# Performance work log

Measured on AMD Instinct MI355X. Metric: run time of the kernel, lower is better.

The kernel has to match this reference:

```python
import jax, jax.numpy as jnp
import numpy as np

N_NODES = 50000
DIM = 64
HEADS = 4
N_EDGES = 800000
NEG_SLOPE = 0.2  # PyG GATConv default


def setup_inputs() -> dict:
    key = jax.random.key(0)
    ks = jax.random.split(key, 8)
    H, C = HEADS, DIM
    embedding = jax.random.normal(ks[0], (N_NODES, DIM), dtype=jnp.float32)
    graph = jax.random.randint(ks[1], (2, N_EDGES), 0, N_NODES, dtype=jnp.int64)
    s = 1.0 / np.sqrt(DIM)
    # GATConv params: shared source/target linear (PyG uses one lin when in_channels is int)
    W = jax.random.normal(ks[2], (DIM, H * C), dtype=jnp.float32) * s
    att_src = jax.random.normal(ks[3], (H, C), dtype=jnp.float32) * s
    att_dst = jax.random.normal(ks[4], (H, C), dtype=jnp.float32) * s
    bias = jnp.zeros((H * C,), dtype=jnp.float32)
    # dense: Linear(dim*heads -> dim)
    dense_w = jax.random.normal(ks[5], (H * C, DIM), dtype=jnp.float32) / np.sqrt(H * C)
    dense_b = jnp.zeros((DIM,), dtype=jnp.float32)
    return {"embedding": embedding, "graph": graph, "W": W, "att_src": att_src,
            "att_dst": att_dst, "bias": bias, "dense_w": dense_w, "dense_b": dense_b}


def reference(embedding, graph, W, att_src, att_dst, bias, dense_w, dense_b):
    N, D = embedding.shape
    H, C = att_src.shape
    # linear projection, per-head view: [N, H, C]
    x = (embedding @ W).reshape(N, H, C)
    # add self loops (PyG default add_self_loops=True)
    ar = jnp.arange(N, dtype=graph.dtype)
    src = jnp.concatenate([graph[0], ar])  # [E+N]
    dst = jnp.concatenate([graph[1], ar])
    # per-node attention logits, gathered per edge
    a_src = jnp.einsum('nhc,hc->nh', x, att_src)  # [N, H]
    a_dst = jnp.einsum('nhc,hc->nh', x, att_dst)
    alpha = jax.nn.leaky_relu(a_src[src] + a_dst[dst], NEG_SLOPE)  # [E, H]
    # segment softmax over destination nodes
    amax = jax.ops.segment_max(alpha, dst, num_segments=N)  # [N, H]
    amax = jnp.where(jnp.isfinite(amax), amax, 0.0)
    ex = jnp.exp(alpha - amax[dst])
    denom = jax.ops.segment_sum(ex, dst, num_segments=N)
    coef = ex / (denom[dst] + 1e-16)  # [E, H]
    # weighted scatter-aggregate of source features
    msg = x[src] * coef[:, :, None]  # [E, H, C]
    agg = jax.ops.segment_sum(msg, dst, num_segments=N)  # [N, H, C]
    gat_out = agg.reshape(N, H * C) + bias  # concat heads + bias
    return gat_out @ dense_w + dense_b  # [N, D]
```

## Files before the change

### kernel.cpp

```cpp
#include <hip/hip_runtime.h>
#include <hip/hip_fp16.h>
#include <cfloat>
#include <cmath>

#define DIM 64
#define HEADS 4
#define NEG 0.2f
#define CAP 64
#define NPART 8
#define BPP 96

typedef int v4i __attribute__((ext_vector_type(4)));

__device__ __forceinline__ float lrelu(float a) { return a > 0.0f ? a : NEG * a; }

__device__ __forceinline__ unsigned pack_half2(float a, float b) {
    return (unsigned)__half_as_ushort(__float2half(a)) |
           ((unsigned)__half_as_ushort(__float2half(b)) << 16);
}

__global__ __launch_bounds__(256) void prep_kernel(
        const float* __restrict__ W, const float* __restrict__ dw,
        const float* __restrict__ att_s, const float* __restrict__ att_d,
        const float* __restrict__ bias, const float* __restrict__ db,
        const float* __restrict__ emb,
        float* __restrict__ M, float* __restrict__ bvec,
        float* __restrict__ a_src, float* __restrict__ a_dst,
        int* __restrict__ cnt, int N) {
    const int b = blockIdx.x, t = threadIdx.x;
    if (b < 64) {
        __shared__ float s_W[256];
        s_W[t] = W[b * 256 + t];
        __syncthreads();
        const int h = t >> 6, j = t & 63;
        float s = 0.f;
        for (int c = 0; c < 64; c++)
            s = fmaf(s_W[h * 64 + c], dw[(h * 64 + c) * 64 + j], s);
        M[b * 256 + t] = s;
    } else if (b == 64) {
        __shared__ float s_p[256];
        const int j = t & 63, kq = t >> 6;
        float p = 0.f;
        for (int k = kq * 64; k < kq * 64 + 64; k++)
            p = fmaf(bias[k], dw[k * 64 + j], p);
        s_p[t] = p;
        __syncthreads();
        if (t < 64)
            bvec[t] = s_p[t] + s_p[64 + t] + s_p[128 + t] + s_p[192 + t] + db[t];
    } else {
        __shared__ float s_e[64 * 68];
        __shared__ float s_vs[256], s_vd[256];
        const int n0 = (b - 65) * 64;
        {
            const int d = t >> 2, h = t & 3;
            const float4* w4 = (const float4*)(W + d * 256 + h * 64);
            const float4* s4 = (const float4*)(att_s + h * 64);
            const float4* d4 = (const float4*)(att_d + h * 64);
            float vs = 0.f, vd = 0.f;
#pragma unroll
            for (int k = 0; k < 16; k++) {
                float4 w = w4[k], as = s4[k], ad = d4[k];
                vs = fmaf(w.x, as.x, fmaf(w.y, as.y, fmaf(w.z, as.z, fmaf(w.w, as.w, vs))));
                vd = fmaf(w.x, ad.x, fmaf(w.y, ad.y, fmaf(w.z, ad.z, fmaf(w.w, ad.w, vd))));
            }
            s_vs[h * 64 + d] = vs;
            s_vd[h * 64 + d] = vd;
        }
#pragma unroll
        for (int r = 0; r < 4; r++) {
            int idx = (r * 256 + t) * 4;
            int i = idx >> 6, d = idx & 63;
            int row = min(n0 + i, N - 1);
            *(float4*)(s_e + i * 68 + d) = *(const float4*)(emb + (size_t)row * 64 + d);
        }
        __syncthreads();
        const int node = t >> 2, h = t & 3;
        const float* er = s_e + node * 68;
        float as = 0.f, ad = 0.f;
#pragma unroll
        for (int g = 0; g < 16; g++) {
            float4 ev = *(const float4*)(er + 4 * g);
            float4 vs = *(const float4*)(s_vs + h * 64 + 4 * g);
            float4 vd = *(const float4*)(s_vd + h * 64 + 4 * g);
            as = fmaf(ev.x, vs.x, fmaf(ev.y, vs.y, fmaf(ev.z, vs.z, fmaf(ev.w, vs.w, as))));
            ad = fmaf(ev.x, vd.x, fmaf(ev.y, vd.y, fmaf(ev.z, vd.z, fmaf(ev.w, vd.w, ad))));
        }
        const int n = n0 + node;
        if (n < N) {
            a_src[(size_t)n * 4 + h] = as;
            a_dst[(size_t)n * 4 + h] = ad;
        }
        if (t < 64 && n0 + t < N) cnt[n0 + t] = 0;
    }
}

__global__ __launch_bounds__(256) void project_kernel(
        const float* __restrict__ emb, const float* __restrict__ M,
        unsigned* __restrict__ y32, int N) {
    __shared__ float s_e[64 * 68];
    const int t = threadIdx.x;
    const int l = t & 63;
    const int wq = __builtin_amdgcn_readfirstlane(t >> 6);
    const int n0 = blockIdx.x * 64;

#pragma unroll
    for (int r = 0; r < 4; r++) {
        int idx = (r * 256 + t) * 4;
        int i = idx >> 6, d = idx & 63;
        int row = min(n0 + i, N - 1);
        *(float4*)(s_e + i * 68 + d) = *(const float4*)(emb + (size_t)row * 64 + d);
    }
    __syncthreads();

    float4 acc[16];
#pragma unroll
    for (int i = 0; i < 16; i++) acc[i] = make_float4(0.f, 0.f, 0.f, 0.f);

    const float* eb = s_e + wq * 16 * 68;

    for (int g = 0; g < 16; g++) {
        const int d0 = g * 4;
        float4 wv0 = *(const float4*)(M + (d0 + 0) * 256 + 4 * l);
        float4 wv1 = *(const float4*)(M + (d0 + 1) * 256 + 4 * l);
        float4 wv2 = *(const float4*)(M + (d0 + 2) * 256 + 4 * l);
        float4 wv3 = *(const float4*)(M + (d0 + 3) * 256 + 4 * l);
#pragma unroll
        for (int i = 0; i < 16; i++) {
            float4 ev = *(const float4*)(eb + i * 68 + d0);
            acc[i].x = fmaf(ev.x, wv0.x, acc[i].x);
            acc[i].y = fmaf(ev.x, wv0.y, acc[i].y);
            acc[i].z = fmaf(ev.x, wv0.z, acc[i].z);
            acc[i].w = fmaf(ev.x, wv0.w, acc[i].w);
            acc[i].x = fmaf(ev.y, wv1.x, acc[i].x);
            acc[i].y = fmaf(ev.y, wv1.y, acc[i].y);
            acc[i].z = fmaf(ev.y, wv1.z, acc[i].z);
            acc[i].w = fmaf(ev.y, wv1.w, acc[i].w);
            acc[i].x = fmaf(ev.z, wv2.x, acc[i].x);
            acc[i].y = fmaf(ev.z, wv2.y, acc[i].y);
            acc[i].z = fmaf(ev.z, wv2.z, acc[i].z);
            acc[i].w = fmaf(ev.z, wv2.w, acc[i].w);
            acc[i].x = fmaf(ev.w, wv3.x, acc[i].x);
            acc[i].y = fmaf(ev.w, wv3.y, acc[i].y);
            acc[i].z = fmaf(ev.w, wv3.z, acc[i].z);
            acc[i].w = fmaf(ev.w, wv3.w, acc[i].w);
        }
    }

#pragma unroll
    for (int i = 0; i < 16; i++) {
        int n = n0 + wq * 16 + i;
        if (n < N) {
            unsigned long long u =
                (unsigned long long)pack_half2(acc[i].x, acc[i].y) |
                ((unsigned long long)pack_half2(acc[i].z, acc[i].w) << 32);
            __builtin_nontemporal_store(u,
                (unsigned long long*)(y32 + (size_t)n * 128 + 2 * l));
        }
    }
}

__global__ __launch_bounds__(256) void fill_kernel(
        const int* __restrict__ gsrc, const int* __restrict__ gdst,
        int* __restrict__ cnt, int* __restrict__ adj, int E, int N) {
    const int t = threadIdx.x;
    const int part = blockIdx.x & (NPART - 1);
    const int slot = blockIdx.x >> 3;
    const int lo = (int)((long long)part * N / NPART);
    const int hi = (int)((long long)(part + 1) * N / NPART);
    const unsigned span = (unsigned)(hi - lo);
    const int quads = (E + 3) >> 2;
    const int stride = BPP * 256;

    for (int q = slot * 256 + t; q < quads; q += stride) {
        const int e0 = q * 4;
        v4i s4, d4;
        if (e0 + 3 < E) {
            d4 = __builtin_nontemporal_load((const v4i*)(gdst + e0));
            s4 = __builtin_nontemporal_load((const v4i*)(gsrc + e0));
        } else {
#pragma unroll
            for (int k = 0; k < 4; k++) {
                const int e = e0 + k;
                d4[k] = (e < E) ? gdst[e] : -1;
                s4[k] = (e < E) ? gsrc[e] : 0;
            }
        }
#pragma unroll
        for (int k = 0; k < 4; k++) {
            const int d = d4[k];
            if ((unsigned)(d - lo) < span) {
                const int pos = atomicAdd(&cnt[d], 1);
                if (pos < CAP) adj[(size_t)d * CAP + pos] = s4[k];
            }
        }
    }
}

__global__ __launch_bounds__(256) void aggregate_kernel(
        const int* __restrict__ cnt, const int* __restrict__ adj,
        const float* __restrict__ a_src, const float* __restrict__ a_dst,
        const unsigned* __restrict__ y32, const float* __restrict__ bvec,
        float* __restrict__ out, int N) {
    const int t = threadIdx.x;
    const int l = t & 63;
    const int dd = blockIdx.x * 4 + (t >> 6);
    if (dd >= N) return;
    const int d = __builtin_amdgcn_readfirstlane(dd);
    const int hl = l >> 4;
    const int lh = l & 48;
    const int deg = min(__builtin_amdgcn_readfirstlane(cnt[d]), CAP);
    const unsigned* yl = y32 + 2 * l;

    int my_src = 0;
    if (l < deg) my_src = adj[(size_t)d * CAP + l];

    const float ad = a_dst[(size_t)d * 4 + hl];

    float pv0, pv1, pv2, pv3;
    {
        const int q = l & 15;
#define PRE_PV(G, PV) {                                                    \
            const int e_ = (G) * 16 + q;                                   \
            const int se_ = __shfl(my_src, e_, 64);                        \
            float pe_ = 0.f;                                               \
            if (e_ < deg)                                                  \
                pe_ = __expf(lrelu(a_src[(size_t)se_ * 4 + hl] + ad));     \
            (PV) = pe_; }
        PRE_PV(0, pv0); PRE_PV(1, pv1); PRE_PV(2, pv2); PRE_PV(3, pv3);
#undef PRE_PV
    }

    float den, ax, ay, az, aw;
    {
        const float p = __expf(lrelu(a_src[(size_t)d * 4 + hl] + ad));
        const uint2 v = *(const uint2*)(yl + (size_t)d * 128);
        const float2 f0 = __half22float2(*(const __half2*)&v.x);
        const float2 f1 = __half22float2(*(const __half2*)&v.y);
        den = p;
        ax = p * f0.x; ay = p * f0.y; az = p * f1.x; aw = p * f1.y;
    }

#define AGG_EDGE(PG, I, J) {                                               \
        const int si_ = __builtin_amdgcn_readlane(my_src, (I));            \
        const float pe_ = __shfl((PG), lh + (J), 64);                      \
        const uint2 vv_ = *(const uint2*)(yl + (size_t)si_ * 128);         \
        const float2 g0_ = __half22float2(*(const __half2*)&vv_.x);        \
        const float2 g1_ = __half22float2(*(const __half2*)&vv_.y);        \
        den += pe_;                                                        \
        ax = fmaf(pe_, g0_.x, ax); ay = fmaf(pe_, g0_.y, ay);              \
        az = fmaf(pe_, g1_.x, az); aw = fmaf(pe_, g1_.y, aw); }

#define AGG_GROUP(G, PG) {                                                 \
        const int base_ = (G) * 16;                                        \
        if (base_ < deg) {                                                 \
            const int mp_ = min(16, ((deg - base_) + 3) & ~3);             \
            _Pragma("unroll 1")                                            \
            for (int j = 0; j < mp_; j += 4) {                             \
                AGG_EDGE(PG, base_ + j + 0, j + 0);                        \
                AGG_EDGE(PG, base_ + j + 1, j + 1);                        \
                AGG_EDGE(PG, base_ + j + 2, j + 2);                        \
                AGG_EDGE(PG, base_ + j + 3, j + 3);                        \
            }                                                              \
        } }

    AGG_GROUP(0, pv0);
    AGG_GROUP(1, pv1);
    AGG_GROUP(2, pv2);
    AGG_GROUP(3, pv3);
#undef AGG_GROUP
#undef AGG_EDGE

    const float inv = 1.0f / (den + 1e-16f);
    float rx = ax * inv, ry = ay * inv, rz = az * inv, rw = aw * inv;
    rx += __shfl_xor(rx, 16, 64); ry += __shfl_xor(ry, 16, 64);
    rz += __shfl_xor(rz, 16, 64); rw += __shfl_xor(rw, 16, 64);
    rx += __shfl_xor(rx, 32, 64); ry += __shfl_xor(ry, 32, 64);
    rz += __shfl_xor(rz, 32, 64); rw += __shfl_xor(rw, 32, 64);
    if (l < 16) {
        float4 bv = *(const float4*)(bvec + 4 * l);
        float4 r;
        r.x = rx + bv.x; r.y = ry + bv.y; r.z = rz + bv.z; r.w = rw + bv.w;
        *(float4*)(out + (size_t)dd * 64 + 4 * l) = r;
    }
}

extern "C" void kernel_launch(void* const* d_in, const int* in_sizes, int n_in,
                              void* d_out, int out_size, void* d_ws, size_t ws_size,
                              hipStream_t stream) {
    const float* emb   = (const float*)d_in[0];
    const int*   graph = (const int*)d_in[1];
    const float* W     = (const float*)d_in[2];
    const float* att_s = (const float*)d_in[3];
    const float* att_d = (const float*)d_in[4];
    const float* bias  = (const float*)d_in[5];
    const float* dw    = (const float*)d_in[6];
    const float* db    = (const float*)d_in[7];
    float* out = (float*)d_out;

    const int N = in_sizes[0] / DIM;
    const int E = in_sizes[1] / 2;
    const int* gsrc = graph;
    const int* gdst = graph + E;

    unsigned* y32  = (unsigned*)d_ws;
    int* adj       = (int*)(y32 + (size_t)N * 128);
    float* a_src   = (float*)(adj + (size_t)N * CAP);
    float* a_dst   = a_src + (size_t)N * 4;
    float* M       = a_dst + (size_t)N * 4;
    float* bvec    = M + 64 * 256;
    int*   cnt     = (int*)(bvec + 64);

    const int PB = (N + 63) / 64;
    const int FILLB = NPART * BPP;

    hipLaunchKernelGGL(prep_kernel, dim3(65 + PB), dim3(256), 0, stream,
                       W, dw, att_s, att_d, bias, db, emb,
                       M, bvec, a_src, a_dst, cnt, N);
    hipLaunchKernelGGL(project_kernel, dim3(PB), dim3(256), 0, stream,
                       emb, M, y32, N);
    hipLaunchKernelGGL(fill_kernel, dim3(FILLB), dim3(256), 0, stream,
                       gsrc, gdst, cnt, adj, E, N);
    hipLaunchKernelGGL(aggregate_kernel, dim3((N + 3) / 4), dim3(256), 0, stream,
                       cnt, adj, a_src, a_dst, y32, bvec, out, N);
}
```

Measured before the change: 228.0 us.

## Aggregate raw fp16 embeddings per head, then apply fused projection after aggregation

Moves the combined W·dense_w projection from before the edge aggregation to after it. The aggregate kernel now gathers 64-dim fp16 embeddings (128 B per source) instead of 256-dim projected features (512 B per source), and writes per-head weighted embeddings to a buffer. A new output GEMM kernel multiplies that buffer by the per-head fused matrix. This cuts gather traffic in the edge loop at the cost of an extra intermediate buffer write/read and a larger post-aggregation GEMM.

```diff
diff --git a/kernel.cpp b/kernel.cpp
--- a/kernel.cpp
+++ b/kernel.cpp
@@ -24,9 +24,9 @@
         const float* __restrict__ att_s, const float* __restrict__ att_d,
         const float* __restrict__ bias, const float* __restrict__ db,
         const float* __restrict__ emb,
-        float* __restrict__ M, float* __restrict__ bvec,
+        __half* __restrict__ M2h, float* __restrict__ bvec,
         float* __restrict__ a_src, float* __restrict__ a_dst,
-        int* __restrict__ cnt, int N) {
+        unsigned* __restrict__ embh, int* __restrict__ cnt, int N) {
     const int b = blockIdx.x, t = threadIdx.x;
     if (b < 64) {
         __shared__ float s_W[256];
@@ -36,7 +36,7 @@
         float s = 0.f;
         for (int c = 0; c < 64; c++)
             s = fmaf(s_W[h * 64 + c], dw[(h * 64 + c) * 64 + j], s);
-        M[b * 256 + t] = s;
+        M2h[(size_t)(h * 64 + b) * 64 + j] = __float2half(s);
     } else if (b == 64) {
         __shared__ float s_p[256];
         const int j = t & 63, kq = t >> 6;
@@ -89,73 +89,17 @@
         if (n < N) {
             a_src[(size_t)n * 4 + h] = as;
             a_dst[(size_t)n * 4 + h] = ad;
+            const float* ep = s_e + node * 68 + h * 16;
+            uint4 u0, u1;
+            u0.x = pack_half2(ep[0],  ep[1]);  u0.y = pack_half2(ep[2],  ep[3]);
+            u0.z = pack_half2(ep[4],  ep[5]);  u0.w = pack_half2(ep[6],  ep[7]);
+            u1.x = pack_half2(ep[8],  ep[9]);  u1.y = pack_half2(ep[10], ep[11]);
+            u1.z = pack_half2(ep[12], ep[13]); u1.w = pack_half2(ep[14], ep[15]);
+            unsigned* dst = embh + (size_t)n * 32 + h * 8;
+            *(uint4*)dst = u0;
+            *(uint4*)(dst + 4) = u1;
         }
         if (t < 64 && n0 + t < N) cnt[n0 + t] = 0;
-    }
-}
-
-__global__ __launch_bounds__(256) void project_kernel(
-        const float* __restrict__ emb, const float* __restrict__ M,
-        unsigned* __restrict__ y32, int N) {
-    __shared__ float s_e[64 * 68];
-    const int t = threadIdx.x;
-    const int l = t & 63;
-    const int wq = __builtin_amdgcn_readfirstlane(t >> 6);
-    const int n0 = blockIdx.x * 64;
-
-#pragma unroll
-    for (int r = 0; r < 4; r++) {
-        int idx = (r * 256 + t) * 4;
-        int i = idx >> 6, d = idx & 63;
-        int row = min(n0 + i, N - 1);
-        *(float4*)(s_e + i * 68 + d) = *(const float4*)(emb + (size_t)row * 64 + d);
-    }
-    __syncthreads();
-
-    float4 acc[16];
-#pragma unroll
-    for (int i = 0; i < 16; i++) acc[i] = make_float4(0.f, 0.f, 0.f, 0.f);
-
-    const float* eb = s_e + wq * 16 * 68;
-
-    for (int g = 0; g < 16; g++) {
-        const int d0 = g * 4;
-        float4 wv0 = *(const float4*)(M + (d0 + 0) * 256 + 4 * l);
-        float4 wv1 = *(const float4*)(M + (d0 + 1) * 256 + 4 * l);
-        float4 wv2 = *(const float4*)(M + (d0 + 2) * 256 + 4 * l);
-        float4 wv3 = *(const float4*)(M + (d0 + 3) * 256 + 4 * l);
-#pragma unroll
-        for (int i = 0; i < 16; i++) {
-            float4 ev = *(const float4*)(eb + i * 68 + d0);
-            acc[i].x = fmaf(ev.x, wv0.x, acc[i].x);
-            acc[i].y = fmaf(ev.x, wv0.y, acc[i].y);
-            acc[i].z = fmaf(ev.x, wv0.z, acc[i].z);
-            acc[i].w = fmaf(ev.x, wv0.w, acc[i].w);
-            acc[i].x = fmaf(ev.y, wv1.x, acc[i].x);
-            acc[i].y = fmaf(ev.y, wv1.y, acc[i].y);
-            acc[i].z = fmaf(ev.y, wv1.z, acc[i].z);
-            acc[i].w = fmaf(ev.y, wv1.w, acc[i].w);
-            acc[i].x = fmaf(ev.z, wv2.x, acc[i].x);
-            acc[i].y = fmaf(ev.z, wv2.y, acc[i].y);
-            acc[i].z = fmaf(ev.z, wv2.z, acc[i].z);
-            acc[i].w = fmaf(ev.z, wv2.w, acc[i].w);
-            acc[i].x = fmaf(ev.w, wv3.x, acc[i].x);
-            acc[i].y = fmaf(ev.w, wv3.y, acc[i].y);
-            acc[i].z = fmaf(ev.w, wv3.z, acc[i].z);
-            acc[i].w = fmaf(ev.w, wv3.w, acc[i].w);
-        }
-    }
-
-#pragma unroll
-    for (int i = 0; i < 16; i++) {
-        int n = n0 + wq * 16 + i;
-        if (n < N) {
-            unsigned long long u =
-                (unsigned long long)pack_half2(acc[i].x, acc[i].y) |
-                ((unsigned long long)pack_half2(acc[i].z, acc[i].w) << 32);
-            __builtin_nontemporal_store(u,
-                (unsigned long long*)(y32 + (size_t)n * 128 + 2 * l));
-        }
     }
 }
 
@@ -199,8 +143,7 @@
 __global__ __launch_bounds__(256) void aggregate_kernel(
         const int* __restrict__ cnt, const int* __restrict__ adj,
         const float* __restrict__ a_src, const float* __restrict__ a_dst,
-        const unsigned* __restrict__ y32, const float* __restrict__ bvec,
-        float* __restrict__ out, int N) {
+        const unsigned* __restrict__ embh, unsigned* __restrict__ zbuf, int N) {
     const int t = threadIdx.x;
     const int l = t & 63;
     const int dd = blockIdx.x * 4 + (t >> 6);
@@ -208,8 +151,9 @@
     const int d = __builtin_amdgcn_readfirstlane(dd);
     const int hl = l >> 4;
     const int lh = l & 48;
+    const int q = l & 15;
     const int deg = min(__builtin_amdgcn_readfirstlane(cnt[d]), CAP);
-    const unsigned* yl = y32 + 2 * l;
+    const unsigned* el = embh + 2 * q;
 
     int my_src = 0;
     if (l < deg) my_src = adj[(size_t)d * CAP + l];
@@ -218,7 +162,6 @@
 
     float pv0, pv1, pv2, pv3;
     {
-        const int q = l & 15;
 #define PRE_PV(G, PV) {                                                    \
             const int e_ = (G) * 16 + q;                                   \
             const int se_ = __shfl(my_src, e_, 64);                        \
@@ -230,25 +173,25 @@
 #undef PRE_PV
     }
 
-    float den, ax, ay, az, aw;
+    float den, zx, zy, zz, zw;
     {
         const float p = __expf(lrelu(a_src[(size_t)d * 4 + hl] + ad));
-        const uint2 v = *(const uint2*)(yl + (size_t)d * 128);
+        const uint2 v = *(const uint2*)(el + (size_t)d * 32);
         const float2 f0 = __half22float2(*(const __half2*)&v.x);
         const float2 f1 = __half22float2(*(const __half2*)&v.y);
         den = p;
-        ax = p * f0.x; ay = p * f0.y; az = p * f1.x; aw = p * f1.y;
+        zx = p * f0.x; zy = p * f0.y; zz = p * f1.x; zw = p * f1.y;
     }
 
 #define AGG_EDGE(PG, I, J) {                                               \
         const int si_ = __builtin_amdgcn_readlane(my_src, (I));            \
         const float pe_ = __shfl((PG), lh + (J), 64);                      \
-        const uint2 vv_ = *(const uint2*)(yl + (size_t)si_ * 128);         \
+        const uint2 vv_ = *(const uint2*)(el + (size_t)si_ * 32);          \
         const float2 g0_ = __half22float2(*(const __half2*)&vv_.x);        \
         const float2 g1_ = __half22float2(*(const __half2*)&vv_.y);        \
         den += pe_;                                                        \
-        ax = fmaf(pe_, g0_.x, ax); ay = fmaf(pe_, g0_.y, ay);              \
-        az = fmaf(pe_, g1_.x, az); aw = fmaf(pe_, g1_.y, aw); }
+        zx = fmaf(pe_, g0_.x, zx); zy = fmaf(pe_, g0_.y, zy);              \
+        zz = fmaf(pe_, g1_.x, zz); zw = fmaf(pe_, g1_.y, zw); }
 
 #define AGG_GROUP(G, PG) {                                                 \
         const int base_ = (G) * 16;                                        \
@@ -271,16 +214,82 @@
 #undef AGG_EDGE
 
     const float inv = 1.0f / (den + 1e-16f);
-    float rx = ax * inv, ry = ay * inv, rz = az * inv, rw = aw * inv;
-    rx += __shfl_xor(rx, 16, 64); ry += __shfl_xor(ry, 16, 64);
-    rz += __shfl_xor(rz, 16, 64); rw += __shfl_xor(rw, 16, 64);
-    rx += __shfl_xor(rx, 32, 64); ry += __shfl_xor(ry, 32, 64);
-    rz += __shfl_xor(rz, 32, 64); rw += __shfl_xor(rw, 32, 64);
-    if (l < 16) {
-        float4 bv = *(const float4*)(bvec + 4 * l);
-        float4 r;
-        r.x = rx + bv.x; r.y = ry + bv.y; r.z = rz + bv.z; r.w = rw + bv.w;
-        *(float4*)(out + (size_t)dd * 64 + 4 * l) = r;
+    uint2 u;
+    u.x = pack_half2(zx * inv, zy * inv);
+    u.y = pack_half2(zz * inv, zw * inv);
+    *(uint2*)(zbuf + (size_t)dd * 128 + 2 * l) = u;
+}
+
+__global__ __launch_bounds__(256) void outgemm_kernel(
+        const unsigned* __restrict__ zbuf, const unsigned* __restrict__ M2u,
+        const float* __restrict__ bvec, float* __restrict__ out, int N) {
+    __shared__ unsigned s_m[8192];
+    __shared__ unsigned s_z[8192];
+    const int t = threadIdx.x;
+    const int n0 = blockIdx.x * 64;
+
+#pragma unroll
+    for (int r = 0; r < 8; r++)
+        *(uint4*)(s_m + (r * 256 + t) * 4) = *(const uint4*)(M2u + (r * 256 + t) * 4);
+#pragma unroll
+    for (int r = 0; r < 8; r++) {
+        const int idx = r * 256 + t;
+        const int row = idx >> 5, c4 = (idx & 31) * 4;
+        const int n = n0 + row;
+        uint4 v = make_uint4(0u, 0u, 0u, 0u);
+        if (n < N) v = *(const uint4*)(zbuf + (size_t)n * 128 + c4);
+        *(uint4*)(s_z + row * 128 + c4) = v;
+    }
+    __syncthreads();
+
+    const int l = t & 63;
+    const int wq = t >> 6;
+    const int g = l >> 4, q = l & 15;
+    const unsigned* zrow = s_z + (wq * 16) * 128 + g * 32;
+
+    float4 acc[16];
+#pragma unroll
+    for (int i = 0; i < 16; i++) acc[i] = make_float4(0.f, 0.f, 0.f, 0.f);
+
+#pragma unroll 2
+    for (int i = 0; i < 32; i++) {
+        const int kk = (i + 8 * g) & 31;
+        const int k = g * 64 + 2 * kk;
+        const uint2 ma = *(const uint2*)(s_m + k * 32 + 2 * q);
+        const uint2 mb = *(const uint2*)(s_m + (k + 1) * 32 + 2 * q);
+        const float2 a0 = __half22float2(*(const __half2*)&ma.x);
+        const float2 a1 = __half22float2(*(const __half2*)&ma.y);
+        const float2 b0 = __half22float2(*(const __half2*)&mb.x);
+        const float2 b1 = __half22float2(*(const __half2*)&mb.y);
+#pragma unroll
+        for (int n = 0; n < 16; n++) {
+            const unsigned zp = zrow[n * 128 + kk];
+            const float2 zf = __half22float2(*(const __half2*)&zp);
+            acc[n].x = fmaf(zf.x, a0.x, acc[n].x);
+            acc[n].y = fmaf(zf.x, a0.y, acc[n].y);
+            acc[n].z = fmaf(zf.x, a1.x, acc[n].z);
+            acc[n].w = fmaf(zf.x, a1.y, acc[n].w);
+            acc[n].x = fmaf(zf.y, b0.x, acc[n].x);
+            acc[n].y = fmaf(zf.y, b0.y, acc[n].y);
+            acc[n].z = fmaf(zf.y, b1.x, acc[n].z);
+            acc[n].w = fmaf(zf.y, b1.y, acc[n].w);
+        }
+    }
+
+    const float4 bv = *(const float4*)(bvec + 4 * q);
+#pragma unroll
+    for (int n = 0; n < 16; n++) {
+        float4 r = acc[n];
+        r.x += __shfl_xor(r.x, 16, 64); r.y += __shfl_xor(r.y, 16, 64);
+        r.z += __shfl_xor(r.z, 16, 64); r.w += __shfl_xor(r.w, 16, 64);
+        r.x += __shfl_xor(r.x, 32, 64); r.y += __shfl_xor(r.y, 32, 64);
+        r.z += __shfl_xor(r.z, 32, 64); r.w += __shfl_xor(r.w, 32, 64);
+        const int nn = n0 + wq * 16 + n;
+        if (l < 16 && nn < N) {
+            float4 o;
+            o.x = r.x + bv.x; o.y = r.y + bv.y; o.z = r.z + bv.z; o.w = r.w + bv.w;
+            *(float4*)(out + (size_t)nn * 64 + 4 * q) = o;
+        }
     }
 }
 
@@ -302,12 +311,13 @@
     const int* gsrc = graph;
     const int* gdst = graph + E;
 
-    unsigned* y32  = (unsigned*)d_ws;
-    int* adj       = (int*)(y32 + (size_t)N * 128);
-    float* a_src   = (float*)(adj + (size_t)N * CAP);
+    unsigned* zbuf = (unsigned*)d_ws;
+    int* adj       = (int*)(zbuf + (size_t)N * 128);
+    unsigned* embh = (unsigned*)(adj + (size_t)N * CAP);
+    float* a_src   = (float*)(embh + (size_t)N * 32);
     float* a_dst   = a_src + (size_t)N * 4;
-    float* M       = a_dst + (size_t)N * 4;
-    float* bvec    = M + 64 * 256;
+    __half* M2h    = (__half*)(a_dst + (size_t)N * 4);
+    float* bvec    = (float*)((unsigned*)M2h + 8192);
     int*   cnt     = (int*)(bvec + 64);
 
     const int PB = (N + 63) / 64;
@@ -315,11 +325,11 @@
 
     hipLaunchKernelGGL(prep_kernel, dim3(65 + PB), dim3(256), 0, stream,
                        W, dw, att_s, att_d, bias, db, emb,
-                       M, bvec, a_src, a_dst, cnt, N);
-    hipLaunchKernelGGL(project_kernel, dim3(PB), dim3(256), 0, stream,
-                       emb, M, y32, N);
+                       M2h, bvec, a_src, a_dst, embh, cnt, N);
     hipLaunchKernelGGL(fill_kernel, dim3(FILLB), dim3(256), 0, stream,
                        gsrc, gdst, cnt, adj, E, N);
     hipLaunchKernelGGL(aggregate_kernel, dim3((N + 3) / 4), dim3(256), 0, stream,
-                       cnt, adj, a_src, a_dst, y32, bvec, out, N);
-}
+                       cnt, adj, a_src, a_dst, embh, zbuf, N);
+    hipLaunchKernelGGL(outgemm_kernel, dim3(PB), dim3(256), 0, stream,
+                       zbuf, (const unsigned*)M2h, bvec, out, N);
+}
```

After: 217.8 us. 1.05x faster.
